# Kernel optimization log

Hardware: AMD Instinct MI355X
Metric: run time of the kernel (lower is better)

Reference implementation:

```python
import jax, jax.numpy as jnp
import numpy as np

B, T, D = 1, 4096, 2048
H, G, K = 16, 4, 128   # query heads, kv heads, head_dim
R = H // G             # n_rep = 4
EPS = 1e-6
SCALE = K ** -0.5


def rms_norm(x, scale):
    var = jnp.mean(x.astype(jnp.float32) ** 2, axis=-1, keepdims=True)
    normed = x * jax.lax.rsqrt(var + EPS)
    return (scale * normed).astype(x.dtype)


def apply_rope(x_BTHK, sin_BTK, cos_BTK):
    half = x_BTHK.shape[-1] // 2
    x1, x2 = x_BTHK[..., :half], x_BTHK[..., half:]
    s = sin_BTK[:, :, None, :]
    c = cos_BTK[:, :, None, :]
    return jnp.concatenate([x1 * c - x2 * s, x2 * c + x1 * s], axis=-1).astype(x_BTHK.dtype)


def setup_inputs() -> dict:
    key = jax.random.key(0)
    ks = jax.random.split(key, 8)
    hidden = jax.random.normal(ks[0], (B, T, D), dtype=jnp.float32)
    # rope angles
    inv_freq = 1.0 / (10000.0 ** (jnp.arange(0, K, 2, dtype=jnp.float32) / K))  # [K/2]
    pos = jnp.arange(T, dtype=jnp.float32)
    ang = pos[:, None] * inv_freq[None, :]          # [T, K/2]
    sin = jnp.broadcast_to(jnp.sin(ang)[None], (B, T, K // 2))
    cos = jnp.broadcast_to(jnp.cos(ang)[None], (B, T, K // 2))
    mask = jnp.broadcast_to(jnp.tril(jnp.ones((T, T), dtype=bool))[None], (B, T, T))
    std = D ** -0.5
    Wq = jax.random.normal(ks[1], (D, H * K), dtype=jnp.float32) * std
    Wk = jax.random.normal(ks[2], (D, G * K), dtype=jnp.float32) * std
    Wv = jax.random.normal(ks[3], (D, G * K), dtype=jnp.float32) * std
    Wo = jax.random.normal(ks[4], (H * K, D), dtype=jnp.float32) * ((H * K) ** -0.5)
    q_scale = jnp.ones((K,), dtype=jnp.float32)
    k_scale = jnp.ones((K,), dtype=jnp.float32)
    return {"hidden_BTD": hidden, "sin_BTK": sin, "cos_BTK": cos, "mask": mask,
            "Wq": Wq, "Wk": Wk, "Wv": Wv, "Wo": Wo,
            "q_scale": q_scale, "k_scale": k_scale}


def reference(hidden_BTD, sin_BTK, cos_BTK, mask, Wq, Wk, Wv, Wo, q_scale, k_scale):
    q = rms_norm((hidden_BTD @ Wq).reshape(B, T, H, K), q_scale)
    k = rms_norm((hidden_BTD @ Wk).reshape(B, T, G, K), k_scale)
    v = (hidden_BTD @ Wv).reshape(B, T, G, K)
    q = apply_rope(q, sin_BTK, cos_BTK)
    k = apply_rope(k, sin_BTK, cos_BTK)
    q_BTGRK = q.reshape(B, T, G, R, K)
    logits = jnp.einsum('BTGRK,BSGK->BTSGR', q_BTGRK, k) * SCALE
    neg = float(jnp.finfo(logits.dtype).min)
    logits = jnp.where(mask[:, :, :, None, None], logits, neg)
    weights = jax.nn.softmax(logits.astype(jnp.float32), axis=2).astype(logits.dtype)
    attn = jnp.einsum('BTSGR,BSGK->BTGRK', weights, v)
    return attn.reshape(B, T, H * K) @ Wo
```

## Files before the change

kernel.cpp:

```cpp
#include <hip/hip_runtime.h>
#include <hip/hip_bf16.h>
#include <stdint.h>

#define T_SEQ 4096
#define KVB 64
#define BM 128
#define BN 128
#define BK 64
#define SCL2 (0.08838834764831845f * 1.44269504088896340f)

typedef unsigned short u16;
typedef __attribute__((ext_vector_type(8))) short s16x8;
typedef __attribute__((ext_vector_type(4))) short s16x4;
typedef __attribute__((ext_vector_type(4))) float f32x4;

__device__ __forceinline__ u16 f2bf(float f) {
  union { float f; unsigned u; } a; a.f = f;
  unsigned r = a.u + 0x7fffu + ((a.u >> 16) & 1u);
  return (u16)(r >> 16);
}
__device__ __forceinline__ float bf2f(u16 b) {
  union { unsigned u; float f; } a; a.u = ((unsigned)b) << 16;
  return a.f;
}
__device__ __forceinline__ unsigned cvtpk(float lo, float hi) {
  unsigned r;
  asm volatile("v_cvt_pk_bf16_f32 %0, %1, %2" : "=v"(r) : "v"(lo), "v"(hi));
  return r;
}

__device__ __forceinline__ void gl_lds16(const void* g, void* l) {
  __builtin_amdgcn_global_load_lds((const __attribute__((address_space(1))) void*)g,
                                   (__attribute__((address_space(3))) void*)l, 16, 0, 0);
}

__global__ __launch_bounds__(256) void k_cvt(const float* __restrict__ in, u16* __restrict__ out) {
  int i = (blockIdx.x * 256 + threadIdx.x) * 8;
  const float4* p = (const float4*)(in + i);
  float4 a = p[0], b = p[1];
  s16x8 o;
  o[0] = (short)f2bf(a.x); o[1] = (short)f2bf(a.y); o[2] = (short)f2bf(a.z); o[3] = (short)f2bf(a.w);
  o[4] = (short)f2bf(b.x); o[5] = (short)f2bf(b.y); o[6] = (short)f2bf(b.z); o[7] = (short)f2bf(b.w);
  *(s16x8*)(out + i) = o;
}

__global__ __launch_bounds__(256) void k_transpose_cvt(const float* __restrict__ in, u16* __restrict__ out,
                                                       int R, int C) {
  __shared__ float tile[32][33];
  int c0 = blockIdx.x * 32, r0 = blockIdx.y * 32;
  int tx = threadIdx.x & 31, ty = threadIdx.x >> 5;
#pragma unroll
  for (int k = 0; k < 4; k++) tile[ty + 8 * k][tx] = in[(size_t)(r0 + ty + 8 * k) * C + c0 + tx];
  __syncthreads();
#pragma unroll
  for (int k = 0; k < 4; k++) out[(size_t)(c0 + ty + 8 * k) * R + r0 + tx] = f2bf(tile[tx][ty + 8 * k]);
}

__global__ __launch_bounds__(256, 2) void k_gemm(const u16* __restrict__ A, const u16* __restrict__ Bt,
                                                 u16* __restrict__ Cq, u16* __restrict__ Ck, u16* __restrict__ Cvt,
                                                 float* __restrict__ Cf, int M, int N, int Kd, int mode) {
  __shared__ u16 SM[BM * BK + BN * BK];
  u16* As = SM;
  u16* Bs = SM + BM * BK;
  int tid = threadIdx.x, lane = tid & 63, w = tid >> 6;
  int g = lane >> 4, r16 = lane & 15;
  int m0 = blockIdx.y * BM, n0 = blockIdx.x * BN;
  int wr = w >> 1, wc = w & 1;
  f32x4 acc[4][4] = {};

  for (int kt = 0; kt < Kd; kt += BK) {
#pragma unroll
    for (int i = 0; i < 4; i++) {
      int idx = i * 256 + tid;
      int row = idx >> 3, c = idx & 7;
      int cs = c ^ (row & 7);
      gl_lds16(A + (size_t)(m0 + row) * Kd + kt + cs * 8, As + (i * 256 + w * 64) * 8);
    }
#pragma unroll
    for (int i = 0; i < 4; i++) {
      int idx = i * 256 + tid;
      int row = idx >> 3, c = idx & 7;
      int cs = c ^ (row & 7);
      gl_lds16(Bt + (size_t)(n0 + row) * Kd + kt + cs * 8, Bs + (i * 256 + w * 64) * 8);
    }
    __syncthreads();
#pragma unroll
    for (int kk = 0; kk < 2; kk++) {
      s16x8 af[4], bfr[4];
#pragma unroll
      for (int mi = 0; mi < 4; mi++) {
        int row = wr * 64 + mi * 16 + r16;
        af[mi] = *(const s16x8*)(As + row * 64 + (((kk * 4 + g) ^ (row & 7)) * 8));
      }
#pragma unroll
      for (int ni = 0; ni < 4; ni++) {
        int row = wc * 64 + ni * 16 + r16;
        bfr[ni] = *(const s16x8*)(Bs + row * 64 + (((kk * 4 + g) ^ (row & 7)) * 8));
      }
#pragma unroll
      for (int mi = 0; mi < 4; mi++)
#pragma unroll
        for (int ni = 0; ni < 4; ni++)
          acc[mi][ni] = __builtin_amdgcn_mfma_f32_16x16x32_bf16(af[mi], bfr[ni], acc[mi][ni], 0, 0, 0);
    }
    __syncthreads();
  }

#pragma unroll
  for (int mi = 0; mi < 4; mi++) {
    int rowb = m0 + wr * 64 + mi * 16 + g * 4;
#pragma unroll
    for (int ni = 0; ni < 4; ni++) {
      int ncol0 = n0 + wc * 64 + ni * 16;
      int col = ncol0 + r16;
      if (mode == 0) {
        if (ncol0 < 2048) {
#pragma unroll
          for (int j = 0; j < 4; j++) Cq[(size_t)(rowb + j) * 2048 + col] = f2bf(acc[mi][ni][j]);
        } else if (ncol0 < 2560) {
#pragma unroll
          for (int j = 0; j < 4; j++) Ck[(size_t)(rowb + j) * 512 + (col - 2048)] = f2bf(acc[mi][ni][j]);
        } else {
          s16x4 pk;
#pragma unroll
          for (int j = 0; j < 4; j++) pk[j] = (short)f2bf(acc[mi][ni][j]);
          *(s16x4*)(Cvt + (size_t)(col - 2560) * T_SEQ + rowb) = pk;
        }
      } else {
#pragma unroll
        for (int j = 0; j < 4; j++) Cf[(size_t)(rowb + j) * N + col] = acc[mi][ni][j];
      }
    }
  }
}

__global__ __launch_bounds__(256) void k_normrope(u16* __restrict__ Q, u16* __restrict__ Kc,
                                                  const float* __restrict__ sinT, const float* __restrict__ cosT,
                                                  const float* __restrict__ qsc, const float* __restrict__ ksc) {
  int t = blockIdx.x;
  int w = threadIdx.x >> 6, lane = threadIdx.x & 63;
  int unit = blockIdx.y * 4 + w;
  u16* base;
  const float* sc;
  float fold;
  if (unit < 16) { base = Q + (size_t)t * 2048 + unit * 128; sc = qsc; fold = SCL2; }
  else { base = Kc + (size_t)t * 512 + (unit - 16) * 128; sc = ksc; fold = 1.0f; }
  float x1 = bf2f(base[lane]), x2 = bf2f(base[lane + 64]);
  float ss = x1 * x1 + x2 * x2;
#pragma unroll
  for (int off = 32; off >= 1; off >>= 1) ss += __shfl_xor(ss, off);
  float rinv = rsqrtf(ss * (1.0f / 128.0f) + 1e-6f);
  float n1 = x1 * rinv * sc[lane], n2 = x2 * rinv * sc[lane + 64];
  float s = sinT[t * 64 + lane], c = cosT[t * 64 + lane];
  base[lane] = f2bf((n1 * c - n2 * s) * fold);
  base[lane + 64] = f2bf((n2 * c + n1 * s) * fold);
}

__global__ __launch_bounds__(256, 2) void k_attn(const u16* __restrict__ Q, const u16* __restrict__ Kc,
                                                 const u16* __restrict__ Vt, u16* __restrict__ O) {
  __shared__ __align__(16) char SMc[73728];
  int tid = threadIdx.x, lane = tid & 63, w = tid >> 6;
  int g = lane >> 4, r16 = lane & 15;
  int qs = w >> 1, ks = w & 1;

  int bid = blockIdx.x;
  int xcd = bid & 7;
  int lid = bid >> 3;
  int h = xcd * 2 + (lid & 1);
  int qb = 63 - (lid >> 1);
  int gh = h >> 2;
  int q0 = qb * 64;
  int qwv = q0 + qs * 32;
  int nt = qb + 1;

  s16x8 qf[2][4];
#pragma unroll
  for (int qc = 0; qc < 2; qc++)
#pragma unroll
    for (int dc = 0; dc < 4; dc++)
      qf[qc][dc] = *(const s16x8*)(Q + (size_t)(qwv + qc * 16 + r16) * 2048 + h * 128 + dc * 32 + g * 8);

  auto STAGE = [&](int bb, int tt) {
    int kv0 = tt * KVB;
    u16* Kb = (u16*)(SMc + bb * 16384);
    u16* Vb = (u16*)(SMc + 32768 + bb * 16384);
#pragma unroll
    for (int i = 0; i < 4; i++) {
      int idx = i * 256 + tid;
      int row = idx >> 4, cc = idx & 15;
      int cs = cc ^ (row & 7);
      gl_lds16(Kc + (size_t)(kv0 + row) * 512 + gh * 128 + cs * 8, Kb + (i * 256 + w * 64) * 8);
    }
#pragma unroll
    for (int i = 0; i < 4; i++) {
      int idx = i * 256 + tid;
      int row = idx >> 3, cc = idx & 7;
      int cs = cc ^ (row & 7);
      gl_lds16(Vt + (size_t)(gh * 128 + row) * T_SEQ + kv0 + cs * 8, Vb + (i * 256 + w * 64) * 8);
    }
  };

  f32x4 acc[2][8] = {};
  float mrun[2] = {-3.0e38f, -3.0e38f};
  float lrun[2] = {0.0f, 0.0f};

  STAGE(0, 0);
  __syncthreads();

  for (int t = 0; t < nt; ++t) {
    int kv0 = t * KVB;
    int bb = t & 1;
    STAGE(bb ^ 1, (t + 1 < nt) ? t + 1 : 0);

    int kvw = kv0 + ks * 32;
    if (kvw <= qwv + 31) {
      u16* Kb = (u16*)(SMc + bb * 16384);
      u16* Vb = (u16*)(SMc + 32768 + bb * 16384);
      char* Pwb = SMc + 65536 + w * 2048;

      f32x4 sv[2][2] = {};
      __builtin_amdgcn_s_setprio(1);
#pragma unroll
      for (int kc = 0; kc < 2; kc++) {
        int krow = ks * 32 + kc * 16 + r16;
#pragma unroll
        for (int dc = 0; dc < 4; dc++) {
          s16x8 kf = *(const s16x8*)((u16*)Kb + krow * 128 + (((dc * 4 + g) ^ (krow & 7)) * 8));
          sv[0][kc] = __builtin_amdgcn_mfma_f32_16x16x32_bf16(kf, qf[0][dc], sv[0][kc], 0, 0, 0);
          sv[1][kc] = __builtin_amdgcn_mfma_f32_16x16x32_bf16(kf, qf[1][dc], sv[1][kc], 0, 0, 0);
        }
      }
      __builtin_amdgcn_s_setprio(0);

#pragma unroll
      for (int qc = 0; qc < 2; qc++) {
        int qg = qwv + qc * 16 + r16;
        bool needmask = (kvw + 31) > (qwv + qc * 16);
        if (needmask) {
#pragma unroll
          for (int kc = 0; kc < 2; kc++)
#pragma unroll
            for (int j2 = 0; j2 < 4; j2++)
              if (kvw + kc * 16 + g * 4 + j2 > qg) sv[qc][kc][j2] = -3.0e38f;
        }
        float mt = sv[qc][0][0];
#pragma unroll
        for (int kc = 0; kc < 2; kc++)
#pragma unroll
          for (int j2 = 0; j2 < 4; j2++) mt = fmaxf(mt, sv[qc][kc][j2]);
        mt = fmaxf(mt, __shfl_xor(mt, 16));
        mt = fmaxf(mt, __shfl_xor(mt, 32));
        if (__any(mt > mrun[qc] + 8.0f)) {
          float mnew = fmaxf(mrun[qc], mt);
          float al = exp2f(mrun[qc] - mnew);
          mrun[qc] = mnew;
          lrun[qc] *= al;
#pragma unroll
          for (int df = 0; df < 8; df++) acc[qc][df] = acc[qc][df] * al;
        }
        float rs = 0.0f;
#pragma unroll
        for (int kc = 0; kc < 2; kc++) {
          float p0 = exp2f(sv[qc][kc][0] - mrun[qc]);
          float p1 = exp2f(sv[qc][kc][1] - mrun[qc]);
          float p2 = exp2f(sv[qc][kc][2] - mrun[qc]);
          float p3 = exp2f(sv[qc][kc][3] - mrun[qc]);
          rs += (p0 + p1) + (p2 + p3);
          uint2 pk;
          pk.x = cvtpk(p0, p1);
          pk.y = cvtpk(p2, p3);
          int unit = ((qc << 2) | (kc << 1) | (g >> 1)) ^ (r16 & 7);
          *(uint2*)(Pwb + r16 * 128 + unit * 16 + (g & 1) * 8) = pk;
        }
        rs += __shfl_xor(rs, 16);
        rs += __shfl_xor(rs, 32);
        lrun[qc] += rs;
      }

      __builtin_amdgcn_s_setprio(1);
      s16x8 pf0 = *(const s16x8*)(Pwb + r16 * 128 + (((0 * 4 + g) ^ (r16 & 7)) * 16));
      s16x8 pf1 = *(const s16x8*)(Pwb + r16 * 128 + (((1 * 4 + g) ^ (r16 & 7)) * 16));
#pragma unroll
      for (int df = 0; df < 8; df++) {
        int vrow = df * 16 + r16;
        s16x8 vf = *(const s16x8*)((u16*)Vb + vrow * 64 + (((ks * 4 + g) ^ (vrow & 7)) * 8));
        acc[0][df] = __builtin_amdgcn_mfma_f32_16x16x32_bf16(vf, pf0, acc[0][df], 0, 0, 0);
        acc[1][df] = __builtin_amdgcn_mfma_f32_16x16x32_bf16(vf, pf1, acc[1][df], 0, 0, 0);
      }
      __builtin_amdgcn_s_setprio(0);
    }
    __syncthreads();
  }

  float* ml = (float*)(SMc + 65536);
  if (g < 2) {
    float mv = g ? mrun[1] : mrun[0];
    float lv = g ? lrun[1] : lrun[0];
    int mi = ((w * 2 + g) * 16 + r16) * 2;
    ml[mi] = mv;
    ml[mi + 1] = lv;
  }
  __syncthreads();
  int pw = w ^ 1;
  float scale[2];
#pragma unroll
  for (int qc = 0; qc < 2; qc++) {
    float pm = ml[((pw * 2 + qc) * 16 + r16) * 2];
    float pl = ml[((pw * 2 + qc) * 16 + r16) * 2 + 1];
    float ms = fmaxf(mrun[qc], pm);
    float aS = exp2f(mrun[qc] - ms);
    float aP = exp2f(pm - ms);
    float ls = lrun[qc] * aS + pl * aP;
    scale[qc] = aS / ls;
  }
  char* obw = SMc + qs * 16384 + ks * 32768;
#pragma unroll
  for (int qc = 0; qc < 2; qc++)
#pragma unroll
    for (int df = 0; df < 8; df++) {
      f32x4 v = acc[qc][df] * scale[qc];
      int r = qc * 16 + r16;
      int u = df * 4 + g;
      int up = u ^ ((r & 7) << 2);
      *(f32x4*)(obw + r * 512 + up * 16) = v;
    }
  __syncthreads();
#pragma unroll
  for (int it = 0; it < 8; it++) {
    int item = it * 256 + tid;
    int qs2 = item >> 10, rem = item & 1023;
    int r = rem >> 5, u = rem & 31;
    int up = u ^ ((r & 7) << 2);
    f32x4 a = *(const f32x4*)(SMc + qs2 * 16384 + r * 512 + up * 16);
    f32x4 b = *(const f32x4*)(SMc + 32768 + qs2 * 16384 + r * 512 + up * 16);
    f32x4 sSum = a + b;
    uint2 pk;
    pk.x = cvtpk(sSum[0], sSum[1]);
    pk.y = cvtpk(sSum[2], sSum[3]);
    *(uint2*)(O + (size_t)(q0 + qs2 * 32 + r) * 2048 + h * 128 + u * 4) = pk;
  }
}

extern "C" void kernel_launch(void* const* d_in, const int* in_sizes, int n_in,
                              void* d_out, int out_size, void* d_ws, size_t ws_size,
                              hipStream_t stream) {
  const float* hidden = (const float*)d_in[0];
  const float* sinT = (const float*)d_in[1];
  const float* cosT = (const float*)d_in[2];
  const float* Wq = (const float*)d_in[4];
  const float* Wk = (const float*)d_in[5];
  const float* Wv = (const float*)d_in[6];
  const float* Wo = (const float*)d_in[7];
  const float* qsc = (const float*)d_in[8];
  const float* ksc = (const float*)d_in[9];
  float* out = (float*)d_out;

  char* ws = (char*)d_ws;
  u16* Xb   = (u16*)(ws + 0);
  u16* Bqkv = (u16*)(ws + 16777216);
  u16* Wot  = (u16*)(ws + 29360128);
  u16* Qraw = (u16*)(ws + 37748736);
  u16* Kraw = (u16*)(ws + 54525952);
  u16* Vt   = (u16*)(ws + 58720256);
  u16* Oat  = (u16*)(ws + 62914560);

  k_cvt<<<dim3(4096), dim3(256), 0, stream>>>(hidden, Xb);
  k_transpose_cvt<<<dim3(64, 64), dim3(256), 0, stream>>>(Wq, Bqkv, 2048, 2048);
  k_transpose_cvt<<<dim3(16, 64), dim3(256), 0, stream>>>(Wk, Bqkv + 2048 * 2048, 2048, 512);
  k_transpose_cvt<<<dim3(16, 64), dim3(256), 0, stream>>>(Wv, Bqkv + 2560 * 2048, 2048, 512);
  k_transpose_cvt<<<dim3(64, 64), dim3(256), 0, stream>>>(Wo, Wot, 2048, 2048);

  k_gemm<<<dim3(24, 32), dim3(256), 0, stream>>>(Xb, Bqkv, Qraw, Kraw, Vt, (float*)nullptr,
                                                 4096, 3072, 2048, 0);
  k_normrope<<<dim3(4096, 5), dim3(256), 0, stream>>>(Qraw, Kraw, sinT, cosT, qsc, ksc);
  k_attn<<<dim3(1024), dim3(256), 0, stream>>>(Qraw, Kraw, Vt, Oat);
  k_gemm<<<dim3(16, 32), dim3(256), 0, stream>>>(Oat, Wot, (u16*)nullptr, (u16*)nullptr, (u16*)nullptr,
                                                 out, 4096, 2048, 2048, 1);
}
```

Measured before the change: 268.3 us.

## Cut attention LDS to 48KB: single-buffer V, register P via shuffles

The attention kernel's shared memory drops from 72KB to 48KB so that three blocks can fit per CU (launch bounds raised to 3). V is single-buffered and loaded after the PV step, behind an extra barrier. The softmax probabilities are rearranged into the MFMA operand layout with cross-lane shuffles instead of going through an LDS scratch buffer. The final merge of the two kv-split halves writes only one half to LDS and has the other half add and store directly. In exchange, each iteration gets one more barrier and V loads are exposed rather than prefetched, and the tighter register budget could cause spills.

```diff
diff --git a/kernel.cpp b/kernel.cpp
--- a/kernel.cpp
+++ b/kernel.cpp
@@ -156,9 +156,9 @@
   base[lane + 64] = f2bf((n2 * c + n1 * s) * fold);
 }
 
-__global__ __launch_bounds__(256, 2) void k_attn(const u16* __restrict__ Q, const u16* __restrict__ Kc,
+__global__ __launch_bounds__(256, 3) void k_attn(const u16* __restrict__ Q, const u16* __restrict__ Kc,
                                                  const u16* __restrict__ Vt, u16* __restrict__ O) {
-  __shared__ __align__(16) char SMc[73728];
+  __shared__ __align__(16) char SMc[49152];
   int tid = threadIdx.x, lane = tid & 63, w = tid >> 6;
   int g = lane >> 4, r16 = lane & 15;
   int qs = w >> 1, ks = w & 1;
@@ -180,10 +180,9 @@
     for (int dc = 0; dc < 4; dc++)
       qf[qc][dc] = *(const s16x8*)(Q + (size_t)(qwv + qc * 16 + r16) * 2048 + h * 128 + dc * 32 + g * 8);
 
-  auto STAGE = [&](int bb, int tt) {
+  auto STAGE_K = [&](int bb, int tt) {
     int kv0 = tt * KVB;
     u16* Kb = (u16*)(SMc + bb * 16384);
-    u16* Vb = (u16*)(SMc + 32768 + bb * 16384);
 #pragma unroll
     for (int i = 0; i < 4; i++) {
       int idx = i * 256 + tid;
@@ -191,6 +190,10 @@
       int cs = cc ^ (row & 7);
       gl_lds16(Kc + (size_t)(kv0 + row) * 512 + gh * 128 + cs * 8, Kb + (i * 256 + w * 64) * 8);
     }
+  };
+  auto STAGE_V = [&](int tt) {
+    int kv0 = tt * KVB;
+    u16* Vb = (u16*)(SMc + 32768);
 #pragma unroll
     for (int i = 0; i < 4; i++) {
       int idx = i * 256 + tid;
@@ -204,20 +207,20 @@
   float mrun[2] = {-3.0e38f, -3.0e38f};
   float lrun[2] = {0.0f, 0.0f};
 
-  STAGE(0, 0);
+  STAGE_K(0, 0);
+  STAGE_V(0);
   __syncthreads();
 
   for (int t = 0; t < nt; ++t) {
     int kv0 = t * KVB;
     int bb = t & 1;
-    STAGE(bb ^ 1, (t + 1 < nt) ? t + 1 : 0);
+    if (t + 1 < nt) STAGE_K(bb ^ 1, t + 1);
 
     int kvw = kv0 + ks * 32;
-    if (kvw <= qwv + 31) {
+    bool live = (kvw <= qwv + 31);
+    s16x8 pfr[2];
+    if (live) {
       u16* Kb = (u16*)(SMc + bb * 16384);
-      u16* Vb = (u16*)(SMc + 32768 + bb * 16384);
-      char* Pwb = SMc + 65536 + w * 2048;
-
       f32x4 sv[2][2] = {};
       __builtin_amdgcn_s_setprio(1);
 #pragma unroll
@@ -225,7 +228,7 @@
         int krow = ks * 32 + kc * 16 + r16;
 #pragma unroll
         for (int dc = 0; dc < 4; dc++) {
-          s16x8 kf = *(const s16x8*)((u16*)Kb + krow * 128 + (((dc * 4 + g) ^ (krow & 7)) * 8));
+          s16x8 kf = *(const s16x8*)(Kb + krow * 128 + (((dc * 4 + g) ^ (krow & 7)) * 8));
           sv[0][kc] = __builtin_amdgcn_mfma_f32_16x16x32_bf16(kf, qf[0][dc], sv[0][kc], 0, 0, 0);
           sv[1][kc] = __builtin_amdgcn_mfma_f32_16x16x32_bf16(kf, qf[1][dc], sv[1][kc], 0, 0, 0);
         }
@@ -258,48 +261,68 @@
 #pragma unroll
           for (int df = 0; df < 8; df++) acc[qc][df] = acc[qc][df] * al;
         }
-        float rs = 0.0f;
-#pragma unroll
-        for (int kc = 0; kc < 2; kc++) {
-          float p0 = exp2f(sv[qc][kc][0] - mrun[qc]);
-          float p1 = exp2f(sv[qc][kc][1] - mrun[qc]);
-          float p2 = exp2f(sv[qc][kc][2] - mrun[qc]);
-          float p3 = exp2f(sv[qc][kc][3] - mrun[qc]);
-          rs += (p0 + p1) + (p2 + p3);
-          uint2 pk;
-          pk.x = cvtpk(p0, p1);
-          pk.y = cvtpk(p2, p3);
-          int unit = ((qc << 2) | (kc << 1) | (g >> 1)) ^ (r16 & 7);
-          *(uint2*)(Pwb + r16 * 128 + unit * 16 + (g & 1) * 8) = pk;
-        }
+        float p00 = exp2f(sv[qc][0][0] - mrun[qc]);
+        float p01 = exp2f(sv[qc][0][1] - mrun[qc]);
+        float p02 = exp2f(sv[qc][0][2] - mrun[qc]);
+        float p03 = exp2f(sv[qc][0][3] - mrun[qc]);
+        float p10 = exp2f(sv[qc][1][0] - mrun[qc]);
+        float p11 = exp2f(sv[qc][1][1] - mrun[qc]);
+        float p12 = exp2f(sv[qc][1][2] - mrun[qc]);
+        float p13 = exp2f(sv[qc][1][3] - mrun[qc]);
+        float rs = ((p00 + p01) + (p02 + p03)) + ((p10 + p11) + (p12 + p13));
         rs += __shfl_xor(rs, 16);
         rs += __shfl_xor(rs, 32);
         lrun[qc] += rs;
-      }
-
+        unsigned w0 = cvtpk(p00, p01);
+        unsigned w1 = cvtpk(p02, p03);
+        unsigned w2 = cvtpk(p10, p11);
+        unsigned w3 = cvtpk(p12, p13);
+        int sA = (g & 1) * 32 + r16;
+        int sB = sA + 16;
+        unsigned e0 = (unsigned)__shfl((int)w0, sA);
+        unsigned e1 = (unsigned)__shfl((int)w1, sA);
+        unsigned e2 = (unsigned)__shfl((int)w0, sB);
+        unsigned e3 = (unsigned)__shfl((int)w1, sB);
+        unsigned f0 = (unsigned)__shfl((int)w2, sA);
+        unsigned f1 = (unsigned)__shfl((int)w3, sA);
+        unsigned f2 = (unsigned)__shfl((int)w2, sB);
+        unsigned f3 = (unsigned)__shfl((int)w3, sB);
+        bool hi = (g & 2) != 0;
+        union { unsigned u[4]; s16x8 v; } pu;
+        pu.u[0] = hi ? f0 : e0;
+        pu.u[1] = hi ? f1 : e1;
+        pu.u[2] = hi ? f2 : e2;
+        pu.u[3] = hi ? f3 : e3;
+        pfr[qc] = pu.v;
+      }
+    }
+    __syncthreads();
+
+    if (live) {
+      u16* Vb = (u16*)(SMc + 32768);
       __builtin_amdgcn_s_setprio(1);
-      s16x8 pf0 = *(const s16x8*)(Pwb + r16 * 128 + (((0 * 4 + g) ^ (r16 & 7)) * 16));
-      s16x8 pf1 = *(const s16x8*)(Pwb + r16 * 128 + (((1 * 4 + g) ^ (r16 & 7)) * 16));
 #pragma unroll
       for (int df = 0; df < 8; df++) {
         int vrow = df * 16 + r16;
-        s16x8 vf = *(const s16x8*)((u16*)Vb + vrow * 64 + (((ks * 4 + g) ^ (vrow & 7)) * 8));
-        acc[0][df] = __builtin_amdgcn_mfma_f32_16x16x32_bf16(vf, pf0, acc[0][df], 0, 0, 0);
-        acc[1][df] = __builtin_amdgcn_mfma_f32_16x16x32_bf16(vf, pf1, acc[1][df], 0, 0, 0);
+        s16x8 vf = *(const s16x8*)(Vb + vrow * 64 + (((ks * 4 + g) ^ (vrow & 7)) * 8));
+        acc[0][df] = __builtin_amdgcn_mfma_f32_16x16x32_bf16(vf, pfr[0], acc[0][df], 0, 0, 0);
+        acc[1][df] = __builtin_amdgcn_mfma_f32_16x16x32_bf16(vf, pfr[1], acc[1][df], 0, 0, 0);
       }
       __builtin_amdgcn_s_setprio(0);
     }
     __syncthreads();
-  }
-
-  float* ml = (float*)(SMc + 65536);
-  if (g < 2) {
-    float mv = g ? mrun[1] : mrun[0];
-    float lv = g ? lrun[1] : lrun[0];
-    int mi = ((w * 2 + g) * 16 + r16) * 2;
-    ml[mi] = mv;
-    ml[mi + 1] = lv;
-  }
+
+    if (t + 1 < nt) STAGE_V(t + 1);
+  }
+
+  float* ml = (float*)(SMc + 32768);
+#pragma unroll
+  for (int qc = 0; qc < 2; qc++)
+    if (g == 0) {
+      int mi = ((w * 2 + qc) * 16 + r16) * 2;
+      ml[mi] = mrun[qc];
+      ml[mi + 1] = lrun[qc];
+    }
   __syncthreads();
   int pw = w ^ 1;
   float scale[2];
@@ -313,31 +336,28 @@
     float ls = lrun[qc] * aS + pl * aP;
     scale[qc] = aS / ls;
   }
-  char* obw = SMc + qs * 16384 + ks * 32768;
-#pragma unroll
-  for (int qc = 0; qc < 2; qc++)
-#pragma unroll
-    for (int df = 0; df < 8; df++) {
-      f32x4 v = acc[qc][df] * scale[qc];
-      int r = qc * 16 + r16;
-      int u = df * 4 + g;
-      int up = u ^ ((r & 7) << 2);
-      *(f32x4*)(obw + r * 512 + up * 16) = v;
-    }
+  if (ks == 0) {
+#pragma unroll
+    for (int qc = 0; qc < 2; qc++)
+#pragma unroll
+      for (int df = 0; df < 8; df++) {
+        f32x4 v = acc[qc][df] * scale[qc];
+        *(f32x4*)(SMc + qs * 16384 + (qc * 16 + r16) * 512 + (((df * 4 + g) ^ (r16 & 7)) * 16)) = v;
+      }
+  }
   __syncthreads();
-#pragma unroll
-  for (int it = 0; it < 8; it++) {
-    int item = it * 256 + tid;
-    int qs2 = item >> 10, rem = item & 1023;
-    int r = rem >> 5, u = rem & 31;
-    int up = u ^ ((r & 7) << 2);
-    f32x4 a = *(const f32x4*)(SMc + qs2 * 16384 + r * 512 + up * 16);
-    f32x4 b = *(const f32x4*)(SMc + 32768 + qs2 * 16384 + r * 512 + up * 16);
-    f32x4 sSum = a + b;
-    uint2 pk;
-    pk.x = cvtpk(sSum[0], sSum[1]);
-    pk.y = cvtpk(sSum[2], sSum[3]);
-    *(uint2*)(O + (size_t)(q0 + qs2 * 32 + r) * 2048 + h * 128 + u * 4) = pk;
+  if (ks == 1) {
+#pragma unroll
+    for (int qc = 0; qc < 2; qc++)
+#pragma unroll
+      for (int df = 0; df < 8; df++) {
+        f32x4 p = *(const f32x4*)(SMc + qs * 16384 + (qc * 16 + r16) * 512 + (((df * 4 + g) ^ (r16 & 7)) * 16));
+        f32x4 o = p + acc[qc][df] * scale[qc];
+        uint2 pk;
+        pk.x = cvtpk(o[0], o[1]);
+        pk.y = cvtpk(o[2], o[3]);
+        *(uint2*)(O + (size_t)(q0 + qs * 32 + qc * 16 + r16) * 2048 + h * 128 + df * 16 + g * 4) = pk;
+      }
   }
 }
 
```

Measured after the change: 301.7 us. 12.4% more time.
